# Kernel optimization log

Hardware: AMD Instinct MI355X
Metric: run time of the kernel (lower is better)

Reference implementation:

```python
import jax, jax.numpy as jnp
import numpy as np

B, T, H = 32, 2048, 1024


def setup_inputs() -> dict:
    key = jax.random.key(0)
    k1, k2, k3, k4, k5 = jax.random.split(key, 5)
    hidden = jax.random.normal(k1, (1, B, H), dtype=jnp.float32)
    encoder_outputs = jax.random.normal(k2, (B, T, H), dtype=jnp.float32)
    # nn.Linear(2H, H): weight [H, 2H], bias [H]
    lim = 1.0 / np.sqrt(2 * H)
    W = jax.random.uniform(k3, (H, 2 * H), minval=-lim, maxval=lim, dtype=jnp.float32)
    b = jax.random.uniform(k4, (H,), minval=-lim, maxval=lim, dtype=jnp.float32)
    stdv = 1.0 / np.sqrt(H)
    v = jax.random.uniform(k5, (H,), minval=-stdv, maxval=stdv, dtype=jnp.float32)
    return {"hidden": hidden, "encoder_outputs": encoder_outputs, "W": W, "b": b, "v": v}


def reference(hidden, encoder_outputs, W, b, v):
    # hidden: [1, B, H] -> broadcast to [B, T, H]
    h = jnp.broadcast_to(jnp.transpose(hidden, (1, 0, 2)), encoder_outputs.shape)
    x = jnp.concatenate([h, encoder_outputs], axis=2)          # [B, T, 2H]
    energy = jnp.tanh(jnp.einsum('btd,hd->bth', x, W) + b)      # [B, T, H]
    scores = jnp.einsum('h,bth->bt', v, energy)[:, None, :]     # [B, 1, T]
    return jax.nn.softmax(scores, axis=2)
```

## Files before the change

kernel.cpp:

```cpp
#include <hip/hip_runtime.h>
#include <hip/hip_bf16.h>

#define H 1024
#define T 2048
#define B 32
#define BM 64
#define BKC 128
#define NCHUNK 8

typedef __attribute__((ext_vector_type(8))) __bf16 bf16x8;
typedef __attribute__((ext_vector_type(16))) float f32x16;
typedef __attribute__((ext_vector_type(8))) unsigned short u16x8;

__device__ __forceinline__ unsigned short f2bf(float f) {
    unsigned int x = __float_as_uint(f);
    x += 0x7fffu + ((x >> 16) & 1u);
    return (unsigned short)(x >> 16);
}

__device__ __forceinline__ float fast_tanh(float x) {
    float t = __expf(2.0f * x);
    return 1.0f - 2.0f * __builtin_amdgcn_rcpf(t + 1.0f);
}

__global__ __launch_bounds__(256) void prep_w_kernel(const float* __restrict__ W,
                                                     unsigned short* __restrict__ Wp) {
    int gid = blockIdx.x * 256 + threadIdx.x;
    int n = gid & (H - 1);
    int kg = gid >> 10;
    const float* srcp = W + (size_t)n * (2 * H) + H + kg * 8;
    float4 f0 = *(const float4*)(srcp);
    float4 f1 = *(const float4*)(srcp + 4);
    u16x8 o;
    o[0] = f2bf(f0.x); o[1] = f2bf(f0.y); o[2] = f2bf(f0.z); o[3] = f2bf(f0.w);
    o[4] = f2bf(f1.x); o[5] = f2bf(f1.y); o[6] = f2bf(f1.z); o[7] = f2bf(f1.w);
    *(u16x8*)(Wp + (size_t)gid * 8) = o;
}

__global__ __launch_bounds__(256) void prep_hp_kernel(const float* __restrict__ hidden,
                                                      const float* __restrict__ W,
                                                      const float* __restrict__ bias,
                                                      float* __restrict__ hp) {
    int b = blockIdx.y;
    int t = threadIdx.x;
    int h = blockIdx.x * 64 + (t >> 2);
    int kq = t & 3;
    const float* hid = hidden + (size_t)b * H + kq * 256;
    const float* wr = W + (size_t)h * (2 * H) + kq * 256;
    float acc = 0.f;
#pragma unroll 4
    for (int d = 0; d < 256; d += 4) {
        float4 wv = *(const float4*)(wr + d);
        float4 hv = *(const float4*)(hid + d);
        acc += wv.x * hv.x + wv.y * hv.y + wv.z * hv.z + wv.w * hv.w;
    }
    acc += __shfl_xor(acc, 1);
    acc += __shfl_xor(acc, 2);
    if (kq == 0) hp[(size_t)b * H + h] = acc + bias[h];
}

#define MFMA32(A, Bv, C) __builtin_amdgcn_mfma_f32_32x32x16_bf16(A, Bv, C, 0, 0, 0)

__global__ __launch_bounds__(1024, 4) void energy_kernel(const float* __restrict__ enc,
                                                         const float* __restrict__ hp,
                                                         const float* __restrict__ vvec,
                                                         const unsigned short* __restrict__ Wp,
                                                         float* __restrict__ scores) {
    __shared__ __align__(16) unsigned short Abuf[2][BM * BKC];
    __shared__ float scpart[16][BM];

    const int tid = threadIdx.x;
    const int b = blockIdx.y;
    const int t0 = blockIdx.x * BM;
    const int wave = tid >> 6;
    const int lane = tid & 63;
    const int l31 = lane & 31;
    const int hi = lane >> 5;

    const int st_row = tid >> 4;
    const int st_kf = tid & 15;
    const float* st_src = enc + ((size_t)b * T + t0 + st_row) * H + st_kf * 8;
    char* Ab0 = (char*)&Abuf[0][0];
    char* st_dst = Ab0 + st_kf * 1024 + (((st_row ^ (st_kf & 7))) << 4);

    const unsigned short* wp_base = Wp + (size_t)(wave * 64 + l31) * 8 + (size_t)hi * (H * 8);

    f32x16 acc00, acc01, acc10, acc11;
#pragma unroll
    for (int i = 0; i < 16; ++i) { acc00[i] = 0.f; acc01[i] = 0.f; acc10[i] = 0.f; acc11[i] = 0.f; }

    const int rv0 = l31;
    const int rv1 = 32 + l31;

    {
        float4 f0 = *(const float4*)(st_src);
        float4 f1 = *(const float4*)(st_src + 4);
        u16x8 o;
        o[0] = f2bf(f0.x); o[1] = f2bf(f0.y); o[2] = f2bf(f0.z); o[3] = f2bf(f0.w);
        o[4] = f2bf(f1.x); o[5] = f2bf(f1.y); o[6] = f2bf(f1.z); o[7] = f2bf(f1.w);
        *(u16x8*)st_dst = o;
    }
    bf16x8 bA0 = *(const bf16x8*)(wp_base);
    bf16x8 bA1 = *(const bf16x8*)(wp_base + 256);
    bf16x8 bB0 = *(const bf16x8*)(wp_base + (size_t)H * 16);
    bf16x8 bB1 = *(const bf16x8*)(wp_base + (size_t)H * 16 + 256);
    __syncthreads();

#define STEP(KI, C0, C1)                                                       \
    {                                                                          \
        const int ks = (KI) * 2 + hi;                                          \
        const char* ap = Ab + ks * 1024;                                       \
        bf16x8 a0 = *(const bf16x8*)(ap + ((rv0 ^ (ks & 7)) << 4));            \
        bf16x8 a1 = *(const bf16x8*)(ap + ((rv1 ^ (ks & 7)) << 4));            \
        __builtin_amdgcn_s_setprio(1);                                         \
        acc00 = MFMA32(a0, C0, acc00);                                         \
        acc01 = MFMA32(a0, C1, acc01);                                         \
        acc10 = MFMA32(a1, C0, acc10);                                         \
        acc11 = MFMA32(a1, C1, acc11);                                         \
        __builtin_amdgcn_s_setprio(0);                                         \
        const int nitw = (j * 8 + (KI) + 2) & 63;                              \
        const unsigned short* bp = wp_base + (size_t)nitw * (H * 16);          \
        C0 = *(const bf16x8*)(bp);                                             \
        C1 = *(const bf16x8*)(bp + 256);                                       \
    }

    for (int j = 0; j < NCHUNK; ++j) {
        float4 f0, f1;
        const bool pfA = (j < NCHUNK - 1);
        if (pfA) {
            const float* p = st_src + (j + 1) * BKC;
            f0 = *(const float4*)(p);
            f1 = *(const float4*)(p + 4);
        }
        const char* Ab = Ab0 + (j & 1) * 16384;
        STEP(0, bA0, bA1)
        STEP(1, bB0, bB1)
        STEP(2, bA0, bA1)
        STEP(3, bB0, bB1)
        STEP(4, bA0, bA1)
        STEP(5, bB0, bB1)
        STEP(6, bA0, bA1)
        STEP(7, bB0, bB1)
        if (pfA) {
            u16x8 o;
            o[0] = f2bf(f0.x); o[1] = f2bf(f0.y); o[2] = f2bf(f0.z); o[3] = f2bf(f0.w);
            o[4] = f2bf(f1.x); o[5] = f2bf(f1.y); o[6] = f2bf(f1.z); o[7] = f2bf(f1.w);
            *(u16x8*)(st_dst + ((j + 1) & 1) * 16384) = o;
        }
        __syncthreads();
    }
#undef STEP

    const size_t bH = (size_t)b * H;
    const int col0 = wave * 64 + l31;
    const int col1 = col0 + 32;
    const float hp0 = hp[bH + col0], hp1 = hp[bH + col1];
    const float v0 = vvec[col0], v1 = vvec[col1];
    float psc[2][16];
#pragma unroll
    for (int r = 0; r < 16; ++r) {
        psc[0][r] = v0 * fast_tanh(acc00[r] + hp0) + v1 * fast_tanh(acc01[r] + hp1);
        psc[1][r] = v0 * fast_tanh(acc10[r] + hp0) + v1 * fast_tanh(acc11[r] + hp1);
    }

#pragma unroll
    for (int rg = 0; rg < 2; ++rg)
#pragma unroll
        for (int r = 0; r < 16; ++r) {
            float s = psc[rg][r];
            s += __shfl_xor(s, 1);
            s += __shfl_xor(s, 2);
            s += __shfl_xor(s, 4);
            s += __shfl_xor(s, 8);
            s += __shfl_xor(s, 16);
            psc[rg][r] = s;
        }
    if (l31 == 0) {
#pragma unroll
        for (int rg = 0; rg < 2; ++rg)
#pragma unroll
            for (int r = 0; r < 16; ++r) {
                int m = rg * 32 + (r & 3) + 8 * (r >> 2) + 4 * hi;
                scpart[wave][m] = psc[rg][r];
            }
    }
    __syncthreads();
    if (tid < BM) {
        float s = 0.f;
#pragma unroll
        for (int w = 0; w < 16; ++w) s += scpart[w][tid];
        scores[(size_t)b * T + t0 + tid] = s;
    }
}

__global__ __launch_bounds__(256) void softmax_kernel(const float* __restrict__ sc,
                                                      float* __restrict__ out) {
    int b = blockIdx.x;
    int tid = threadIdx.x;
    int wave = tid >> 6, lane = tid & 63;
    const float* row = sc + (size_t)b * T;
    float vals[8];
    float m = -1e30f;
#pragma unroll
    for (int i = 0; i < 8; ++i) { vals[i] = row[tid + 256 * i]; m = fmaxf(m, vals[i]); }
#pragma unroll
    for (int s = 1; s < 64; s <<= 1) m = fmaxf(m, __shfl_xor(m, s));
    __shared__ float red[4];
    __shared__ float red2[4];
    if (lane == 0) red[wave] = m;
    __syncthreads();
    m = fmaxf(fmaxf(red[0], red[1]), fmaxf(red[2], red[3]));
    float sum = 0.f;
#pragma unroll
    for (int i = 0; i < 8; ++i) { vals[i] = expf(vals[i] - m); sum += vals[i]; }
#pragma unroll
    for (int s = 1; s < 64; s <<= 1) sum += __shfl_xor(sum, s);
    if (lane == 0) red2[wave] = sum;
    __syncthreads();
    sum = red2[0] + red2[1] + red2[2] + red2[3];
    float inv = 1.0f / sum;
#pragma unroll
    for (int i = 0; i < 8; ++i) out[(size_t)b * T + tid + 256 * i] = vals[i] * inv;
}

extern "C" void kernel_launch(void* const* d_in, const int* in_sizes, int n_in,
                              void* d_out, int out_size, void* d_ws, size_t ws_size,
                              hipStream_t stream) {
    (void)in_sizes; (void)n_in; (void)out_size; (void)ws_size;
    const float* hidden = (const float*)d_in[0];
    const float* enc    = (const float*)d_in[1];
    const float* W      = (const float*)d_in[2];
    const float* bias   = (const float*)d_in[3];
    const float* v      = (const float*)d_in[4];
    float* out = (float*)d_out;

    unsigned short* Wp = (unsigned short*)d_ws;
    float* hp = (float*)((char*)d_ws + 2 * 1024 * 1024);
    float* sc = (float*)((char*)d_ws + 2 * 1024 * 1024 + 128 * 1024);

    prep_w_kernel<<<dim3(512), dim3(256), 0, stream>>>(W, Wp);
    prep_hp_kernel<<<dim3(16, B), dim3(256), 0, stream>>>(hidden, W, bias, hp);
    energy_kernel<<<dim3(T / BM, B), dim3(1024), 0, stream>>>(enc, hp, v, Wp, sc);
    softmax_kernel<<<dim3(B), dim3(256), 0, stream>>>(sc, out);
}
```

Before: 226.1 us.

## Interleave per-step barriers with LDS waits to ping-pong waves across MFMA phases

Replaces the single end-of-chunk __syncthreads with an s_barrier, an explicit lgkmcnt wait and a sched_barrier before each MFMA group. The fp32-to-bf16 A-tile staging is moved inside the first and last phase. The last chunk now also loads and stores a wrapped, unused tile, which keeps the code branch-free. The goal is to keep waves in lockstep so LDS reads and MFMAs overlap across waves, at the cost of eight barriers per chunk instead of one.

```diff
diff --git a/kernel.cpp b/kernel.cpp
--- a/kernel.cpp
+++ b/kernel.cpp
@@ -106,12 +106,27 @@
     bf16x8 bB1 = *(const bf16x8*)(wp_base + (size_t)H * 16 + 256);
     __syncthreads();
 
-#define STEP(KI, C0, C1)                                                       \
+#define PH(KI, C0, C1)                                                         \
     {                                                                          \
         const int ks = (KI) * 2 + hi;                                          \
         const char* ap = Ab + ks * 1024;                                       \
         bf16x8 a0 = *(const bf16x8*)(ap + ((rv0 ^ (ks & 7)) << 4));            \
         bf16x8 a1 = *(const bf16x8*)(ap + ((rv1 ^ (ks & 7)) << 4));            \
+        if ((KI) == 0) {                                                       \
+            f0 = *(const float4*)(psrc);                                       \
+            f1 = *(const float4*)(psrc + 4);                                   \
+        }                                                                      \
+        if ((KI) == 7) {                                                       \
+            u16x8 o;                                                           \
+            o[0] = f2bf(f0.x); o[1] = f2bf(f0.y); o[2] = f2bf(f0.z); o[3] = f2bf(f0.w); \
+            o[4] = f2bf(f1.x); o[5] = f2bf(f1.y); o[6] = f2bf(f1.z); o[7] = f2bf(f1.w); \
+            *(u16x8*)wdst = o;                                                 \
+            asm volatile("s_waitcnt lgkmcnt(0)" ::: "memory");                 \
+            __builtin_amdgcn_sched_barrier(0);                                 \
+        }                                                                      \
+        __builtin_amdgcn_s_barrier();                                          \
+        asm volatile("s_waitcnt lgkmcnt(0)" ::: "memory");                     \
+        __builtin_amdgcn_sched_barrier(0);                                     \
         __builtin_amdgcn_s_setprio(1);                                         \
         acc00 = MFMA32(a0, C0, acc00);                                         \
         acc01 = MFMA32(a0, C1, acc01);                                         \
@@ -125,31 +140,20 @@
     }
 
     for (int j = 0; j < NCHUNK; ++j) {
+        const char* Ab = Ab0 + (j & 1) * 16384;
+        char* wdst = st_dst + ((j + 1) & 1) * 16384;
+        const float* psrc = st_src + (size_t)((j + 1) & 7) * BKC;
         float4 f0, f1;
-        const bool pfA = (j < NCHUNK - 1);
-        if (pfA) {
-            const float* p = st_src + (j + 1) * BKC;
-            f0 = *(const float4*)(p);
-            f1 = *(const float4*)(p + 4);
-        }
-        const char* Ab = Ab0 + (j & 1) * 16384;
-        STEP(0, bA0, bA1)
-        STEP(1, bB0, bB1)
-        STEP(2, bA0, bA1)
-        STEP(3, bB0, bB1)
-        STEP(4, bA0, bA1)
-        STEP(5, bB0, bB1)
-        STEP(6, bA0, bA1)
-        STEP(7, bB0, bB1)
-        if (pfA) {
-            u16x8 o;
-            o[0] = f2bf(f0.x); o[1] = f2bf(f0.y); o[2] = f2bf(f0.z); o[3] = f2bf(f0.w);
-            o[4] = f2bf(f1.x); o[5] = f2bf(f1.y); o[6] = f2bf(f1.z); o[7] = f2bf(f1.w);
-            *(u16x8*)(st_dst + ((j + 1) & 1) * 16384) = o;
-        }
-        __syncthreads();
-    }
-#undef STEP
+        PH(0, bA0, bA1)
+        PH(1, bB0, bB1)
+        PH(2, bA0, bA1)
+        PH(3, bB0, bB1)
+        PH(4, bA0, bA1)
+        PH(5, bB0, bB1)
+        PH(6, bA0, bA1)
+        PH(7, bB0, bB1)
+    }
+#undef PH
 
     const size_t bH = (size_t)b * H;
     const int col0 = wave * 64 + l31;
```

Result: slower. 241.4 us (+6.7%).
